# Performance work log

Hardware: AMD Instinct MI355X
Metric: run time of the kernel (lower is better)

Reference implementation:

```python
import jax, jax.numpy as jnp
import numpy as np

B, S, H = 2, 2048, 1024
NH = 16
HD = H // NH  # 64


def setup_inputs() -> dict:
    key = jax.random.key(0)
    ks = jax.random.split(key, 12)
    s = 1.0 / np.sqrt(H)
    return {
        "x_q": jax.random.normal(ks[0], (B, S, H), jnp.float32),
        "x_k": jax.random.normal(ks[1], (B, S, H), jnp.float32),
        "x_v": jax.random.normal(ks[2], (B, S, H), jnp.float32),
        "attention_mask": jax.random.randint(ks[3], (B, S), 0, 2, jnp.int32),
        "Wq": jax.random.normal(ks[4], (H, H), jnp.float32) * s,
        "bq": jnp.zeros((H,), jnp.float32),
        "Wk": jax.random.normal(ks[5], (H, H), jnp.float32) * s,
        "bk": jnp.zeros((H,), jnp.float32),
        "Wv": jax.random.normal(ks[6], (H, H), jnp.float32) * s,
        "bv": jnp.zeros((H,), jnp.float32),
        "Wo": jax.random.normal(ks[7], (H, H), jnp.float32) * s,
        "bo": jnp.zeros((H,), jnp.float32),
    }


def reference(x_q, x_k, x_v, attention_mask, Wq, bq, Wk, bk, Wv, bv, Wo, bo):
    b, s, h = x_q.shape
    # projections
    q = x_q @ Wq + bq
    k = x_k @ Wk + bk
    v = x_v @ Wv + bv
    # [B, NH, S, HD]
    q = q.reshape(b, s, NH, HD).transpose(0, 2, 1, 3)
    k = k.reshape(b, s, NH, HD).transpose(0, 2, 1, 3)
    v = v.reshape(b, s, NH, HD).transpose(0, 2, 1, 3)
    scores = jnp.einsum("bhqd,bhkd->bhqk", q, k) / jnp.sqrt(jnp.float32(HD))
    # key-padding mask: 1 -> keep (0 bias), else -inf; broadcast [B,1,1,S]
    bias = jnp.where(attention_mask == 1, 0.0, -jnp.inf).astype(scores.dtype)
    scores = scores + bias[:, None, None, :]
    attn = jax.nn.softmax(scores, axis=-1)
    # dropout prob = 0.0 (eval / deterministic): identity
    out = jnp.einsum("bhqk,bhkd->bhqd", attn, v)
    out = out.transpose(0, 2, 1, 3).reshape(b, s, h)
    return out @ Wo + bo
```

## Files before the change

### kernel.cpp

```cpp
#include <hip/hip_runtime.h>

#define DEVI static __device__ __forceinline__

typedef unsigned short u16;
typedef unsigned int u32;
typedef __attribute__((ext_vector_type(8))) __bf16 bf16x8;
typedef __attribute__((ext_vector_type(8))) short short8;
typedef __attribute__((ext_vector_type(4))) float f32x4;
typedef __attribute__((ext_vector_type(16))) float f32x16;
typedef __attribute__((ext_vector_type(4))) u32 u32x4;

DEVI u16 f2bf(float f) {
  union { float f; u32 u; } v; v.f = f;
  u32 r = v.u + 0x7fffu + ((v.u >> 16) & 1u);
  return (u16)(r >> 16);
}

DEVI u16 bfc(float f) {
  union { __bf16 b; u16 u; } v; v.b = (__bf16)f; return v.u;
}

DEVI void gload16(const void* g, void* l) {
  __builtin_amdgcn_global_load_lds(
      (const __attribute__((address_space(1))) void*)g,
      (__attribute__((address_space(3))) void*)l,
      16, 0, 0);
}

__global__ void k_maskbias(const int* __restrict__ m, float* __restrict__ bias, int n) {
  int i = blockIdx.x * blockDim.x + threadIdx.x;
  if (i < n) bias[i] = (m[i] == 1) ? 0.f : -1e30f;
}

__global__ void k_transcvt4(const float* __restrict__ W0, const float* __restrict__ W1,
                            const float* __restrict__ W2, const float* __restrict__ W3,
                            u16* __restrict__ Wtb) {
  const int z = blockIdx.z;
  const float* W = (z == 0) ? W0 : ((z == 1) ? W1 : ((z == 2) ? W2 : W3));
  u16* Wt = Wtb + (size_t)z * 1024 * 1024;
  __shared__ float tl[32][33];
  const int n0 = blockIdx.x * 32, k0 = blockIdx.y * 32;
  const int tx = threadIdx.x, ty = threadIdx.y;
#pragma unroll
  for (int r = ty; r < 32; r += 8)
    tl[r][tx] = W[(size_t)(k0 + r) * 1024 + n0 + tx];
  __syncthreads();
#pragma unroll
  for (int r = ty; r < 32; r += 8)
    Wt[(size_t)(n0 + r) * 1024 + k0 + tx] = f2bf(tl[tx][r]);
}

DEVI void store1(u16* C, size_t i, float v) { C[i] = f2bf(v); }
DEVI void store1(float* C, size_t i, float v) { C[i] = v; }

template <typename OutT, bool CVTA>
__global__ __launch_bounds__(256, 2) void k_gemm_bt(
    const u16* __restrict__ Ab, long aZ,
    const float* __restrict__ Af0, const float* __restrict__ Af1,
    const float* __restrict__ Af2,
    const u16* __restrict__ Btbase, long bZ,
    const float* __restrict__ bias0, const float* __restrict__ bias1,
    const float* __restrict__ bias2,
    float s0, float s1, float s2,
    OutT* __restrict__ Cbase, long cZ, u16* __restrict__ Vt,
    int M, int N, int K) {
  const int z = blockIdx.z;
  const u16* A  = Ab + (size_t)z * aZ;
  const float* Af = (z == 0) ? Af0 : ((z == 1) ? Af1 : Af2);
  const u16* Bt = Btbase + (size_t)z * bZ;
  OutT* C = Cbase + (size_t)z * cZ;
  const float* bias = (z == 0) ? bias0 : ((z == 1) ? bias1 : bias2);
  const float scl = (z == 0) ? s0 : ((z == 1) ? s1 : s2);

  __shared__ u16 lsA[128 * 32];
  __shared__ u16 lsB[128 * 32];

  const int t = threadIdx.x;
  const int w = t >> 6, ln = t & 63;
  const int l15 = ln & 15, lhi = ln >> 4;
  const int wr = w >> 1, wc = w & 1;
  const int m0 = blockIdx.x * 128, n0 = blockIdx.y * 128;

  f32x4 acc[4][4] = {};

  for (int kt = 0; kt < K; kt += 32) {
#pragma unroll
    for (int i = 0; i < 2; ++i) {
      const int li = i * 256 + t;
      const int row = li >> 2, cb = (li & 3) << 3;
      if constexpr (CVTA) {
        const float* ap = Af + (size_t)(m0 + row) * K + kt + cb;
        const float4 f0 = *reinterpret_cast<const float4*>(ap);
        const float4 f1 = *reinterpret_cast<const float4*>(ap + 4);
        union { u16 us[8]; short8 s8; } u;
        u.us[0] = bfc(f0.x); u.us[1] = bfc(f0.y); u.us[2] = bfc(f0.z); u.us[3] = bfc(f0.w);
        u.us[4] = bfc(f1.x); u.us[5] = bfc(f1.y); u.us[6] = bfc(f1.z); u.us[7] = bfc(f1.w);
        *reinterpret_cast<short8*>((char*)lsA + (size_t)li * 16) = u.s8;
      } else {
        gload16(A + (size_t)(m0 + row) * K + kt + cb,
                (char*)lsA + (i * 256 + w * 64) * 16);
      }
      gload16(Bt + (size_t)(n0 + row) * K + kt + cb,
              (char*)lsB + (i * 256 + w * 64) * 16);
    }
    __syncthreads();

    bf16x8 af[4], bf_[4];
#pragma unroll
    for (int m = 0; m < 4; ++m)
      af[m] = *reinterpret_cast<const bf16x8*>(
          &lsA[(wr * 64 + m * 16 + l15) * 32 + lhi * 8]);
#pragma unroll
    for (int n = 0; n < 4; ++n)
      bf_[n] = *reinterpret_cast<const bf16x8*>(
          &lsB[(wc * 64 + n * 16 + l15) * 32 + lhi * 8]);
#pragma unroll
    for (int m = 0; m < 4; ++m)
#pragma unroll
      for (int n = 0; n < 4; ++n)
        acc[m][n] = __builtin_amdgcn_mfma_f32_16x16x32_bf16(af[m], bf_[n], acc[m][n], 0, 0, 0);
    __syncthreads();
  }

  if (Vt != nullptr && z == 2) {
#pragma unroll
    for (int n = 0; n < 4; ++n) {
      const int c = n0 + wc * 64 + n * 16 + l15;
      const float bv = bias[c];
#pragma unroll
      for (int m = 0; m < 4; ++m) {
        const int r = m0 + wr * 64 + m * 16 + lhi * 4;
        ushort4 s4;
#pragma unroll
        for (int j = 0; j < 4; ++j) ((u16*)&s4)[j] = f2bf(acc[m][n][j] + bv);
        *reinterpret_cast<ushort4*>(
            &Vt[((size_t)((r >> 11) * 1024 + c)) * 2048 + (r & 2047)]) = s4;
      }
    }
    return;
  }

#pragma unroll
  for (int n = 0; n < 4; ++n) {
    const int c = n0 + wc * 64 + n * 16 + l15;
    const float bv = bias[c];
#pragma unroll
    for (int m = 0; m < 4; ++m)
#pragma unroll
      for (int j = 0; j < 4; ++j) {
        const int r = m0 + wr * 64 + m * 16 + lhi * 4 + j;
        store1(C, (size_t)r * N + c, (acc[m][n][j] + bv) * scl);
      }
  }
}

__global__ __launch_bounds__(256, 2) void k_attn(
    const u16* __restrict__ Q, const u16* __restrict__ K, const u16* __restrict__ Vt,
    const float* __restrict__ MB, u16* __restrict__ O) {
  __shared__ u16 lsK[3][64][72];
  __shared__ u16 lsV[2][64][72];

  const int t = threadIdx.x, w = t >> 6, ln = t & 63;
  const int l31 = ln & 31, h = ln >> 5, h8 = h * 8;
  const int fid = blockIdx.x;
  const int xcd = fid & 7, slot = fid >> 3;
  const int pair = xcd * 4 + (slot >> 4);
  const int qt = slot & 15;
  const int hh = pair & 15, b = pair >> 4;

  const size_t rowQ = (size_t)b * 2048 + qt * 128 + w * 32;
  const int hc = hh * 64;

  const int srow = t >> 3, scol = (t & 7) << 3;
  const u16* Kg = K + ((size_t)b * 2048 + srow) * 1024 + hc + scol;
  const int half = t & 1;
  const int g16 = ((t & 7) >> 1) << 4;
  const u16* VgA = Vt + ((size_t)(b * 1024 + hc) + srow) * 2048 + g16 + 4 * half;
  const float* MBb = MB + b * 2048;

  bf16x8 qb[4];
#pragma unroll
  for (int ks = 0; ks < 4; ++ks)
    qb[ks] = *reinterpret_cast<const bf16x8*>(
        &Q[(rowQ + l31) * 1024 + hc + ks * 16 + h8]);

  f32x16 o[2];
#pragma unroll
  for (int i = 0; i < 16; ++i) { o[0][i] = 0.f; o[1][i] = 0.f; }
  float mrow = -1e30f, lsum = 0.f;

#pragma unroll
  for (int p = 0; p < 3; ++p) {
    const short8 a = *reinterpret_cast<const short8*>(Kg + (size_t)(p * 64) * 1024);
    const short8 c = *reinterpret_cast<const short8*>(Kg + (size_t)(p * 64 + 32) * 1024);
    *reinterpret_cast<short8*>(&lsK[p][srow][scol]) = a;
    *reinterpret_cast<short8*>(&lsK[p][32 + srow][scol]) = c;
  }
#pragma unroll
  for (int p = 0; p < 2; ++p) {
    const ushort4 a = *reinterpret_cast<const ushort4*>(VgA + p * 64);
    const ushort4 b4 = *reinterpret_cast<const ushort4*>(VgA + p * 64 + 8);
    const ushort4 c = *reinterpret_cast<const ushort4*>(VgA + 32 * 2048 + p * 64);
    const ushort4 d = *reinterpret_cast<const ushort4*>(VgA + 32 * 2048 + p * 64 + 8);
    *reinterpret_cast<ushort4*>(&lsV[p][srow][scol]) = a;
    *reinterpret_cast<ushort4*>(&lsV[p][srow][scol + 4]) = b4;
    *reinterpret_cast<ushort4*>(&lsV[p][32 + srow][scol]) = c;
    *reinterpret_cast<ushort4*>(&lsV[p][32 + srow][scol + 4]) = d;
  }
  __syncthreads();

  f32x16 stA[2], stB[2];
#pragma unroll
  for (int f = 0; f < 2; ++f)
#pragma unroll
    for (int rg = 0; rg < 4; ++rg) {
      const f32x4 bv = *reinterpret_cast<const f32x4*>(&MBb[f * 32 + rg * 8 + h * 4]);
#pragma unroll
      for (int jj = 0; jj < 4; ++jj) stA[f][rg * 4 + jj] = bv[jj];
    }
#pragma unroll
  for (int ks = 0; ks < 4; ++ks) {
    const bf16x8 kb0 = *reinterpret_cast<const bf16x8*>(&lsK[0][l31][ks * 16 + h8]);
    const bf16x8 kb1 = *reinterpret_cast<const bf16x8*>(&lsK[0][32 + l31][ks * 16 + h8]);
    stA[0] = __builtin_amdgcn_mfma_f32_32x32x16_bf16(kb0, qb[ks], stA[0], 0, 0, 0);
    stA[1] = __builtin_amdgcn_mfma_f32_32x32x16_bf16(kb1, qb[ks], stA[1], 0, 0, 0);
  }

#define ATTN_BODY(T, CUR, NXT, SW)                                                  \
  {                                                                                 \
    const int tK = ((T) + 3) & 31, tV = ((T) + 2) & 31, tB = ((T) + 1) & 31;        \
    const short8 rk0 = *reinterpret_cast<const short8*>(Kg + (size_t)(tK * 64) * 1024); \
    const short8 rk1 = *reinterpret_cast<const short8*>(Kg + (size_t)(tK * 64 + 32) * 1024); \
    const ushort4 rv0a = *reinterpret_cast<const ushort4*>(VgA + tV * 64);          \
    const ushort4 rv0b = *reinterpret_cast<const ushort4*>(VgA + tV * 64 + 8);      \
    const ushort4 rv1a = *reinterpret_cast<const ushort4*>(VgA + 32 * 2048 + tV * 64); \
    const ushort4 rv1b = *reinterpret_cast<const ushort4*>(VgA + 32 * 2048 + tV * 64 + 8); \
    const int sK = ((SW) == 2) ? 0 : (SW) + 1;                                      \
    _Pragma("unroll")                                                               \
    for (int f = 0; f < 2; ++f)                                                     \
      _Pragma("unroll")                                                             \
      for (int rg = 0; rg < 4; ++rg) {                                              \
        const f32x4 bv = *reinterpret_cast<const f32x4*>(                           \
            &MBb[tB * 64 + f * 32 + rg * 8 + h * 4]);                               \
        _Pragma("unroll")                                                           \
        for (int jj = 0; jj < 4; ++jj) NXT[f][rg * 4 + jj] = bv[jj];                \
      }                                                                             \
    __builtin_amdgcn_s_setprio(1);                                                  \
    _Pragma("unroll")                                                               \
    for (int ks = 0; ks < 4; ++ks) {                                                \
      const bf16x8 kb0 = *reinterpret_cast<const bf16x8*>(&lsK[sK][l31][ks * 16 + h8]); \
      const bf16x8 kb1 = *reinterpret_cast<const bf16x8*>(&lsK[sK][32 + l31][ks * 16 + h8]); \
      NXT[0] = __builtin_amdgcn_mfma_f32_32x32x16_bf16(kb0, qb[ks], NXT[0], 0, 0, 0); \
      NXT[1] = __builtin_amdgcn_mfma_f32_32x32x16_bf16(kb1, qb[ks], NXT[1], 0, 0, 0); \
    }                                                                               \
    __builtin_amdgcn_s_setprio(0);                                                  \
    float tm = CUR[0][0];                                                           \
    _Pragma("unroll")                                                               \
    for (int f = 0; f < 2; ++f)                                                     \
      _Pragma("unroll")                                                             \
      for (int i = 0; i < 16; ++i) tm = fmaxf(tm, CUR[f][i]);                       \
    tm = fmaxf(tm, __shfl_xor(tm, 32, 64));                                         \
    const bool trig = tm > mrow + 8.f;                                              \
    if (__any(trig)) {                                                              \
      const float al = trig ? __builtin_amdgcn_exp2f(mrow - tm) : 1.f;              \
      if (trig) mrow = tm;                                                          \
      lsum *= al;                                                                   \
      _Pragma("unroll")                                                             \
      for (int f = 0; f < 2; ++f)                                                   \
        _Pragma("unroll")                                                           \
        for (int i = 0; i < 16; ++i) o[f][i] *= al;                                 \
    }                                                                               \
    float rs = 0.f;                                                                 \
    _Pragma("unroll")                                                               \
    for (int f = 0; f < 2; ++f)                                                     \
      _Pragma("unroll")                                                             \
      for (int i = 0; i < 16; ++i) {                                                \
        const float p = __builtin_amdgcn_exp2f(CUR[f][i] - mrow);                   \
        CUR[f][i] = p;                                                              \
        rs += p;                                                                    \
      }                                                                             \
    rs += __shfl_xor(rs, 32, 64);                                                   \
    lsum += rs;                                                                     \
    __builtin_amdgcn_s_setprio(1);                                                  \
    _Pragma("unroll")                                                               \
    for (int f = 0; f < 2; ++f) {                                                   \
      u32 pk[8];                                                                    \
      _Pragma("unroll")                                                             \
      for (int i = 0; i < 8; ++i)                                                   \
        pk[i] = (u32)bfc(CUR[f][2 * i]) | ((u32)bfc(CUR[f][2 * i + 1]) << 16);      \
      _Pragma("unroll")                                                             \
      for (int s = 0; s < 2; ++s) {                                                 \
        u32x4 pw;                                                                   \
        pw[0] = pk[4 * s + 0]; pw[1] = pk[4 * s + 1];                               \
        pw[2] = pk[4 * s + 2]; pw[3] = pk[4 * s + 3];                               \
        const bf16x8 pb = __builtin_bit_cast(bf16x8, pw);                           \
        const int ks = f * 2 + s;                                                   \
        _Pragma("unroll")                                                           \
        for (int df2 = 0; df2 < 2; ++df2) {                                         \
          const bf16x8 vt = *reinterpret_cast<const bf16x8*>(                       \
              &lsV[(T) & 1][df2 * 32 + l31][ks * 16 + h8]);                         \
          o[df2] = __builtin_amdgcn_mfma_f32_32x32x16_bf16(vt, pb, o[df2], 0, 0, 0); \
        }                                                                           \
      }                                                                             \
    }                                                                               \
    __builtin_amdgcn_s_setprio(0);                                                  \
    __syncthreads();                                                                \
    *reinterpret_cast<short8*>(&lsK[SW][srow][scol]) = rk0;                         \
    *reinterpret_cast<short8*>(&lsK[SW][32 + srow][scol]) = rk1;                    \
    *reinterpret_cast<ushort4*>(&lsV[(T) & 1][srow][scol]) = rv0a;                  \
    *reinterpret_cast<ushort4*>(&lsV[(T) & 1][srow][scol + 4]) = rv0b;              \
    *reinterpret_cast<ushort4*>(&lsV[(T) & 1][32 + srow][scol]) = rv1a;             \
    *reinterpret_cast<ushort4*>(&lsV[(T) & 1][32 + srow][scol + 4]) = rv1b;         \
  }

  int sw = 0;
  for (int t2 = 0; t2 < 32; t2 += 2) {
    ATTN_BODY(t2, stA, stB, sw);
    sw = (sw == 2) ? 0 : sw + 1;
    ATTN_BODY(t2 + 1, stB, stA, sw);
    sw = (sw == 2) ? 0 : sw + 1;
  }
#undef ATTN_BODY

  const float inv = 1.f / lsum;
#pragma unroll
  for (int df2 = 0; df2 < 2; ++df2)
#pragma unroll
    for (int rg = 0; rg < 4; ++rg) {
      ushort4 s4;
      s4.x = bfc(o[df2][rg * 4 + 0] * inv);
      s4.y = bfc(o[df2][rg * 4 + 1] * inv);
      s4.z = bfc(o[df2][rg * 4 + 2] * inv);
      s4.w = bfc(o[df2][rg * 4 + 3] * inv);
      *reinterpret_cast<ushort4*>(
          &O[(rowQ + l31) * 1024 + hc + df2 * 32 + rg * 8 + h * 4]) = s4;
    }
}

extern "C" void kernel_launch(void* const* d_in, const int* in_sizes, int n_in,
                              void* d_out, int out_size, void* d_ws, size_t ws_size,
                              hipStream_t stream) {
  const float* x_q = (const float*)d_in[0];
  const float* x_k = (const float*)d_in[1];
  const float* x_v = (const float*)d_in[2];
  const int*   msk = (const int*)d_in[3];
  const float* Wq  = (const float*)d_in[4];
  const float* bq  = (const float*)d_in[5];
  const float* Wk  = (const float*)d_in[6];
  const float* bk  = (const float*)d_in[7];
  const float* Wv  = (const float*)d_in[8];
  const float* bv  = (const float*)d_in[9];
  const float* Wo  = (const float*)d_in[10];
  const float* bo  = (const float*)d_in[11];

  const size_t NTOK = 4096, H = 1024;
  u16* wt   = (u16*)d_ws;
  u16* qkv  = wt  + 4 * H * H;
  u16* aout = qkv + 3 * NTOK * H;
  float* mb = (float*)(aout + NTOK * H);
  u16* vtb  = qkv + 2 * NTOK * H;

  k_maskbias<<<dim3(16), dim3(256), 0, stream>>>(msk, mb, 4096);
  k_transcvt4<<<dim3(32, 32, 4), dim3(32, 8), 0, stream>>>(Wq, Wk, Wv, Wo, wt);

  const float qscale = 0.125f * 1.4426950408889634f;
  k_gemm_bt<u16, true><<<dim3(32, 8, 3), dim3(256), 0, stream>>>(
      nullptr, 0L, x_q, x_k, x_v, wt, (long)(H * H), bq, bk, bv,
      qscale, 1.f, 1.f,
      qkv, (long)(NTOK * H), vtb, 4096, 1024, 1024);

  k_attn<<<dim3(512), dim3(256), 0, stream>>>(
      qkv, qkv + NTOK * H, vtb, mb, aout);

  k_gemm_bt<float, false><<<dim3(32, 8, 1), dim3(256), 0, stream>>>(
      aout, 0L, nullptr, nullptr, nullptr, wt + 3 * H * H, 0L, bo, bo, bo,
      1.f, 1.f, 1.f,
      (float*)d_out, 0L, nullptr, 4096, 1024, 1024);
}
```

Measured before the change: 137.1 us.

## Merge prep kernels, prefetch fp32 A tiles, narrow output GEMM tile, defer row-sum shuffle

Folds the mask-bias kernel into the weight transpose/convert kernel as an extra z-slice, saving one launch. The QKV GEMM now issues the fp32 activation loads for the next k-tile into registers before the barrier, so global latency overlaps the current MFMA work. The output projection GEMM uses a 64-wide N tile, giving twice as many blocks for better CU fill. In attention the cross-half row-sum shuffle moves out of the inner loop to a single shuffle at the end. The costs are more registers for the prefetch buffers and many mostly idle blocks in the merged prep grid.

New measurement: 130.3 us. 5.0% less time.

```diff
diff --git a/kernel.cpp b/kernel.cpp
--- a/kernel.cpp
+++ b/kernel.cpp
@@ -27,15 +27,19 @@
       16, 0, 0);
 }
 
-__global__ void k_maskbias(const int* __restrict__ m, float* __restrict__ bias, int n) {
-  int i = blockIdx.x * blockDim.x + threadIdx.x;
-  if (i < n) bias[i] = (m[i] == 1) ? 0.f : -1e30f;
-}
-
-__global__ void k_transcvt4(const float* __restrict__ W0, const float* __restrict__ W1,
-                            const float* __restrict__ W2, const float* __restrict__ W3,
-                            u16* __restrict__ Wtb) {
+__global__ void k_prep(const float* __restrict__ W0, const float* __restrict__ W1,
+                       const float* __restrict__ W2, const float* __restrict__ W3,
+                       u16* __restrict__ Wtb,
+                       const int* __restrict__ msk, float* __restrict__ bias) {
   const int z = blockIdx.z;
+  if (z == 4) {
+    if (blockIdx.x < 16 && blockIdx.y == 0) {
+      const int tid = threadIdx.y * 32 + threadIdx.x;
+      const int i = blockIdx.x * 256 + tid;
+      bias[i] = (msk[i] == 1) ? 0.f : -1e30f;
+    }
+    return;
+  }
   const float* W = (z == 0) ? W0 : ((z == 1) ? W1 : ((z == 2) ? W2 : W3));
   u16* Wt = Wtb + (size_t)z * 1024 * 1024;
   __shared__ float tl[32][33];
@@ -53,7 +57,7 @@
 DEVI void store1(u16* C, size_t i, float v) { C[i] = f2bf(v); }
 DEVI void store1(float* C, size_t i, float v) { C[i] = v; }
 
-template <typename OutT, bool CVTA>
+template <typename OutT, bool CVTA, int BN>
 __global__ __launch_bounds__(256, 2) void k_gemm_bt(
     const u16* __restrict__ Ab, long aZ,
     const float* __restrict__ Af0, const float* __restrict__ Af1,
@@ -72,16 +76,29 @@
   const float* bias = (z == 0) ? bias0 : ((z == 1) ? bias1 : bias2);
   const float scl = (z == 0) ? s0 : ((z == 1) ? s1 : s2);
 
+  constexpr int NF = BN / 32;
   __shared__ u16 lsA[128 * 32];
-  __shared__ u16 lsB[128 * 32];
+  __shared__ u16 lsB[BN * 32];
 
   const int t = threadIdx.x;
   const int w = t >> 6, ln = t & 63;
   const int l15 = ln & 15, lhi = ln >> 4;
   const int wr = w >> 1, wc = w & 1;
-  const int m0 = blockIdx.x * 128, n0 = blockIdx.y * 128;
-
-  f32x4 acc[4][4] = {};
+  const int m0 = blockIdx.x * 128, n0 = blockIdx.y * BN;
+
+  f32x4 acc[4][NF] = {};
+
+  float4 pA0[2], pA1[2];
+  if constexpr (CVTA) {
+#pragma unroll
+    for (int i = 0; i < 2; ++i) {
+      const int li = i * 256 + t;
+      const int row = li >> 2, cb = (li & 3) << 3;
+      const float* ap = Af + (size_t)(m0 + row) * K + cb;
+      pA0[i] = *reinterpret_cast<const float4*>(ap);
+      pA1[i] = *reinterpret_cast<const float4*>(ap + 4);
+    }
+  }
 
   for (int kt = 0; kt < K; kt += 32) {
 #pragma unroll
@@ -89,60 +106,78 @@
       const int li = i * 256 + t;
       const int row = li >> 2, cb = (li & 3) << 3;
       if constexpr (CVTA) {
-        const float* ap = Af + (size_t)(m0 + row) * K + kt + cb;
-        const float4 f0 = *reinterpret_cast<const float4*>(ap);
-        const float4 f1 = *reinterpret_cast<const float4*>(ap + 4);
         union { u16 us[8]; short8 s8; } u;
-        u.us[0] = bfc(f0.x); u.us[1] = bfc(f0.y); u.us[2] = bfc(f0.z); u.us[3] = bfc(f0.w);
-        u.us[4] = bfc(f1.x); u.us[5] = bfc(f1.y); u.us[6] = bfc(f1.z); u.us[7] = bfc(f1.w);
+        u.us[0] = bfc(pA0[i].x); u.us[1] = bfc(pA0[i].y);
+        u.us[2] = bfc(pA0[i].z); u.us[3] = bfc(pA0[i].w);
+        u.us[4] = bfc(pA1[i].x); u.us[5] = bfc(pA1[i].y);
+        u.us[6] = bfc(pA1[i].z); u.us[7] = bfc(pA1[i].w);
         *reinterpret_cast<short8*>((char*)lsA + (size_t)li * 16) = u.s8;
       } else {
         gload16(A + (size_t)(m0 + row) * K + kt + cb,
                 (char*)lsA + (i * 256 + w * 64) * 16);
       }
+    }
+#pragma unroll
+    for (int i = 0; i < BN / 64; ++i) {
+      const int li = i * 256 + t;
+      const int row = li >> 2, cb = (li & 3) << 3;
       gload16(Bt + (size_t)(n0 + row) * K + kt + cb,
               (char*)lsB + (i * 256 + w * 64) * 16);
     }
+    if constexpr (CVTA) {
+      if (kt + 32 < K) {
+#pragma unroll
+        for (int i = 0; i < 2; ++i) {
+          const int li = i * 256 + t;
+          const int row = li >> 2, cb = (li & 3) << 3;
+          const float* ap = Af + (size_t)(m0 + row) * K + kt + 32 + cb;
+          pA0[i] = *reinterpret_cast<const float4*>(ap);
+          pA1[i] = *reinterpret_cast<const float4*>(ap + 4);
+        }
+      }
+    }
     __syncthreads();
 
-    bf16x8 af[4], bf_[4];
+    bf16x8 af[4], bf_[NF];
 #pragma unroll
     for (int m = 0; m < 4; ++m)
       af[m] = *reinterpret_cast<const bf16x8*>(
           &lsA[(wr * 64 + m * 16 + l15) * 32 + lhi * 8]);
 #pragma unroll
-    for (int n = 0; n < 4; ++n)
+    for (int n = 0; n < NF; ++n)
       bf_[n] = *reinterpret_cast<const bf16x8*>(
-          &lsB[(wc * 64 + n * 16 + l15) * 32 + lhi * 8]);
+          &lsB[(wc * (BN / 2) + n * 16 + l15) * 32 + lhi * 8]);
 #pragma unroll
     for (int m = 0; m < 4; ++m)
 #pragma unroll
-      for (int n = 0; n < 4; ++n)
+      for (int n = 0; n < NF; ++n)
         acc[m][n] = __builtin_amdgcn_mfma_f32_16x16x32_bf16(af[m], bf_[n], acc[m][n], 0, 0, 0);
     __syncthreads();
   }
 
-  if (Vt != nullptr && z == 2) {
-#pragma unroll
-    for (int n = 0; n < 4; ++n) {
-      const int c = n0 + wc * 64 + n * 16 + l15;
-      const float bv = bias[c];
-#pragma unroll
-      for (int m = 0; m < 4; ++m) {
-        const int r = m0 + wr * 64 + m * 16 + lhi * 4;
-        ushort4 s4;
-#pragma unroll
-        for (int j = 0; j < 4; ++j) ((u16*)&s4)[j] = f2bf(acc[m][n][j] + bv);
-        *reinterpret_cast<ushort4*>(
-            &Vt[((size_t)((r >> 11) * 1024 + c)) * 2048 + (r & 2047)]) = s4;
+  if constexpr (BN == 128) {
+    if (Vt != nullptr && z == 2) {
+#pragma unroll
+      for (int n = 0; n < NF; ++n) {
+        const int c = n0 + wc * 64 + n * 16 + l15;
+        const float bv = bias[c];
+#pragma unroll
+        for (int m = 0; m < 4; ++m) {
+          const int r = m0 + wr * 64 + m * 16 + lhi * 4;
+          ushort4 s4;
+#pragma unroll
+          for (int j = 0; j < 4; ++j) ((u16*)&s4)[j] = f2bf(acc[m][n][j] + bv);
+          *reinterpret_cast<ushort4*>(
+              &Vt[((size_t)((r >> 11) * 1024 + c)) * 2048 + (r & 2047)]) = s4;
+        }
       }
-    }
-    return;
-  }
-
-#pragma unroll
-  for (int n = 0; n < 4; ++n) {
-    const int c = n0 + wc * 64 + n * 16 + l15;
+      return;
+    }
+  }
+
+#pragma unroll
+  for (int n = 0; n < NF; ++n) {
+    const int c = n0 + wc * (BN / 2) + n * 16 + l15;
     const float bv = bias[c];
 #pragma unroll
     for (int m = 0; m < 4; ++m)
@@ -279,7 +314,6 @@
         CUR[f][i] = p;                                                              \
         rs += p;                                                                    \
       }                                                                             \
-    rs += __shfl_xor(rs, 32, 64);                                                   \
     lsum += rs;                                                                     \
     __builtin_amdgcn_s_setprio(1);                                                  \
     _Pragma("unroll")                                                               \
@@ -322,7 +356,8 @@
   }
 #undef ATTN_BODY
 
-  const float inv = 1.f / lsum;
+  const float ltot = lsum + __shfl_xor(lsum, 32, 64);
+  const float inv = 1.f / ltot;
 #pragma unroll
   for (int df2 = 0; df2 < 2; ++df2)
 #pragma unroll
@@ -360,11 +395,10 @@
   float* mb = (float*)(aout + NTOK * H);
   u16* vtb  = qkv + 2 * NTOK * H;
 
-  k_maskbias<<<dim3(16), dim3(256), 0, stream>>>(msk, mb, 4096);
-  k_transcvt4<<<dim3(32, 32, 4), dim3(32, 8), 0, stream>>>(Wq, Wk, Wv, Wo, wt);
+  k_prep<<<dim3(32, 32, 5), dim3(32, 8), 0, stream>>>(Wq, Wk, Wv, Wo, wt, msk, mb);
 
   const float qscale = 0.125f * 1.4426950408889634f;
-  k_gemm_bt<u16, true><<<dim3(32, 8, 3), dim3(256), 0, stream>>>(
+  k_gemm_bt<u16, true, 128><<<dim3(32, 8, 3), dim3(256), 0, stream>>>(
       nullptr, 0L, x_q, x_k, x_v, wt, (long)(H * H), bq, bk, bv,
       qscale, 1.f, 1.f,
       qkv, (long)(NTOK * H), vtb, 4096, 1024, 1024);
@@ -372,7 +406,7 @@
   k_attn<<<dim3(512), dim3(256), 0, stream>>>(
       qkv, qkv + NTOK * H, vtb, mb, aout);
 
-  k_gemm_bt<float, false><<<dim3(32, 8, 1), dim3(256), 0, stream>>>(
+  k_gemm_bt<float, false, 64><<<dim3(32, 16, 1), dim3(256), 0, stream>>>(
       aout, 0L, nullptr, nullptr, nullptr, wt + 3 * H * H, 0L, bo, bo, bo,
       1.f, 1.f, 1.f,
       (float*)d_out, 0L, nullptr, 4096, 1024, 1024);
```
